# Optimization experiments

Hardware: AMD Instinct MI355X
Metric: run time of the kernel (lower is better)

The kernel has to match this reference:

```python
import jax, jax.numpy as jnp
import numpy as np

N, C, H, W = 8, 32, 48, 48
S, K, OC = 2, 3, 32  # scale_int, kernel_size, out_channels
HID = 256
FEAT = C * K * K  # 288


def setup_inputs() -> dict:
    key = jax.random.key(0)
    ks = jax.random.split(key, 5)
    F_LR = jax.random.normal(ks[0], (N, C, H, W), dtype=jnp.float32)
    v = jax.random.normal(ks[1], (H * S * W * S, 3), dtype=jnp.float32)
    w1 = jax.random.normal(ks[2], (3, HID), dtype=jnp.float32) * 0.2
    b1 = jnp.zeros((HID,), dtype=jnp.float32)
    w2 = jax.random.normal(ks[3], (HID, FEAT * OC), dtype=jnp.float32) * 0.02
    b2 = jnp.zeros((FEAT * OC,), dtype=jnp.float32)
    return {"F_LR": F_LR, "v": v, "w1": w1, "b1": b1, "w2": w2, "b2": b2}


def _unfold(x, k):
    # torch F.unfold(x, k, padding=1): (N, C*k*k, H*W), channel-major then (ki,kj)
    n, c, h, w = x.shape
    xp = jnp.pad(x, ((0, 0), (0, 0), (1, 1), (1, 1)))
    cols = [xp[:, :, i:i + h, j:j + w] for i in range(k) for j in range(k)]
    p = jnp.stack(cols, axis=2)  # (N, C, k*k, H, W)
    return p.reshape(n, c * k * k, h * w)


def reference(F_LR, v, w1, b1, w2, b2):
    n = F_LR.shape[0]
    # weight prediction MLP
    hmid = jax.nn.relu(v @ w1 + b1)
    W_pred = hmid @ w2 + b2  # (H*S*W*S, C*K*K*OC)
    # reshape like torch: view(H,S,W,S,FEAT,OC).permute(1,3,0,2,4,5) -> (S*S, H*W, FEAT, OC)
    Wt = (W_pred.reshape(H, S, W, S, FEAT, OC)
          .transpose(1, 3, 0, 2, 4, 5)
          .reshape(S * S, H * W, FEAT, OC))
    # add_dimensions replicates F_LR S*S times, so patches are shared across p
    pat = _unfold(F_LR, K)  # (N, FEAT, H*W)
    # per-pixel tiny matmul: out[n,p,l,o] = sum_f pat[n,f,l] * Wt[p,l,f,o]
    out = jnp.einsum('nfl,plfo->nplo', pat, Wt)  # (N, S*S, H*W, OC)
    # assemble upsampled image: p=(sh,sw), pixel (h*S+sh, w*S+sw)
    out = (out.reshape(n, S, S, H, W, OC)
           .transpose(0, 5, 3, 1, 4, 2)
           .reshape(n, OC, S * H, S * W))
    # integer scale => create_mask is all-True, masked_select is identity
    return out
```

## Files before the change

### kernel.cpp

```cpp
#include <hip/hip_runtime.h>
#include <hip/hip_bf16.h>

#define NN    8
#define CC    32
#define HH    48
#define WW    48
#define OCC   32
#define HID   256
#define FEAT  288
#define RTOT  9216
#define COLS  9216
#define XUP   96
#define YUP   96
#define OUTSZ (NN*OCC*XUP*YUP)

using bf16x8 = __attribute__((ext_vector_type(8))) __bf16;
using bf16x4 = __attribute__((ext_vector_type(4))) __bf16;
using f32x4  = __attribute__((ext_vector_type(4))) float;

#define GLOAD_LDS16(gp, lp)                                                        \
  __builtin_amdgcn_global_load_lds((const __attribute__((address_space(1))) void*)(gp), \
                                   (__attribute__((address_space(3))) void*)(lp), 16, 0, 0)

__global__ void prep_hmid(const float* __restrict__ v, const float* __restrict__ w1,
                          const float* __restrict__ b1, __hip_bfloat16* __restrict__ hmidp) {
  int r = blockIdx.x;
  int t = threadIdx.x;
  float v0 = v[r*3+0], v1 = v[r*3+1], v2 = v[r*3+2];
  float val = v0*w1[t] + v1*w1[HID+t] + v2*w1[2*HID+t] + b1[t];
  val = fmaxf(val, 0.0f);
  int dst = ((r>>4)*8 + (t>>5))*512 + ((t>>3)&3)*128 + (r&15)*8 + (t&7);
  hmidp[dst] = __float2bfloat16(val);
}

__global__ void prep_w2(const float* __restrict__ w2, __hip_bfloat16* __restrict__ w2p) {
  int idx = blockIdx.x*256 + threadIdx.x;
  int k   = idx / COLS;
  int col = idx % COLS;
  float val = w2[idx];
  int colchunk = col >> 7;
  int cg   = (col >> 4) & 7;
  int lane = (((k>>3)&3)<<4) | (col & 15);
  int kb   = k >> 5;
  int i    = k & 7;
  int dst  = (((colchunk*8 + kb)*8 + cg)*64 + lane)*8 + i;
  w2p[dst] = __float2bfloat16(val);
}

__launch_bounds__(256, 2)
__global__ void fused_main(const float* __restrict__ F_LR,
                           const __hip_bfloat16* __restrict__ hmidp,
                           const __hip_bfloat16* __restrict__ w2p,
                           const float* __restrict__ b2,
                           float* __restrict__ outp,
                           int G, int nch) {
  __shared__ __align__(16) __bf16 pat[CC][3][18][NN];
  __shared__ __align__(16) float  wc[4*OCC*32];
  __shared__ __align__(16) __bf16 Bring[4*4096];
  __shared__ __align__(16) float  biasb[256];
  __shared__ __align__(16) char   dummy[2048];

  const int tid  = threadIdx.x;
  const int lane = tid & 63;
  const int wv   = tid >> 6;
  const int blk  = blockIdx.x;
  int rowtile, g;
  if (G == 2) {
    int xcd = blk & 7;
    int j   = blk >> 3;
    g       = xcd & 1;
    rowtile = (xcd >> 1)*72 + j;
  } else {
    rowtile = blk;
    g       = 0;
  }
  const int X  = rowtile / 3;
  const int Yh = rowtile - X*3;
  const int h  = X >> 1;
  const int w0 = Yh * 16;
  const int l15 = lane & 15;
  const int qt  = lane >> 4;
  const int oc  = lane & 31;
  const int nh  = lane >> 5;
  const int NT = nch*8;

  const char* w2base = (const char*)w2p + (size_t)g*nch*65536;
  char* BringB = (char*)Bring;
  auto stage_any = [&](int t) {
    if (t < NT) {
      const char* src = w2base + (size_t)t*8192 + wv*2048 + lane*16;
      char* dst = BringB + (t&3)*8192 + wv*2048;
      GLOAD_LDS16(src, dst);
      GLOAD_LDS16(src + 1024, dst + 1024);
    } else {
      const char* src = w2base + wv*2048 + lane*16;
      GLOAD_LDS16(src, (char*)dummy);
      GLOAD_LDS16(src + 1024, (char*)dummy + 1024);
    }
  };
  stage_any(0); stage_any(1); stage_any(2);
  asm volatile("" ::: "memory");

  bf16x8 a[2][8];
  {
    const bf16x8* ap = reinterpret_cast<const bf16x8*>(hmidp) + (size_t)rowtile*1024 + lane;
    #pragma unroll
    for (int mg = 0; mg < 2; ++mg)
      #pragma unroll
      for (int kb = 0; kb < 8; ++kb) a[mg][kb] = ap[(mg*8 + kb)*64];
  }

  {
    const int n = tid >> 5, c = tid & 31;
    const float* fsrc = F_LR + ((size_t)(n*CC + c)*HH)*WW;
    #pragma unroll
    for (int ki = 0; ki < 3; ++ki) {
      int hh = h - 1 + ki;
      bool hok = (unsigned)hh < (unsigned)HH;
      #pragma unroll
      for (int wi = 0; wi < 18; ++wi) {
        int ww = w0 - 1 + wi;
        float val = (hok && (unsigned)ww < (unsigned)WW) ? fsrc[hh*WW + ww] : 0.f;
        pat[c][ki][wi][n] = (__bf16)val;
      }
    }
  }
  asm volatile("s_waitcnt lgkmcnt(0)" ::: "memory");
  __builtin_amdgcn_sched_barrier(0);
  __builtin_amdgcn_s_barrier();

  float oacc[8][4];
  #pragma unroll
  for (int i = 0; i < 8; ++i)
    { oacc[i][0]=0.f; oacc[i][1]=0.f; oacc[i][2]=0.f; oacc[i][3]=0.f; }

  for (int ch = 0; ch < nch; ++ch) {
    if ((ch & 1) == 0) {
      const char* bsrc = (const char*)(b2 + (size_t)(g*nch + ch)*128) + lane*16;
      GLOAD_LDS16(bsrc, (char*)biasb);
    }

    f32x4 acc00 = {0,0,0,0}, acc01 = {0,0,0,0}, acc10 = {0,0,0,0}, acc11 = {0,0,0,0};

    #pragma unroll
    for (int s = 0; s < 8; ++s) {
      const int t = ch*8 + s;
      asm volatile("s_waitcnt vmcnt(4)" ::: "memory");
      const char* bufp = BringB + (size_t)(t&3)*8192 + wv*2048;
      bf16x8 b0 = *(const bf16x8*)(bufp + lane*16);
      bf16x8 b1 = *(const bf16x8*)(bufp + 1024 + lane*16);
      stage_any(t + 3);
      acc00 = __builtin_amdgcn_mfma_f32_16x16x32_bf16(a[0][s], b0, acc00, 0,0,0);
      acc01 = __builtin_amdgcn_mfma_f32_16x16x32_bf16(a[0][s], b1, acc01, 0,0,0);
      acc10 = __builtin_amdgcn_mfma_f32_16x16x32_bf16(a[1][s], b0, acc10, 0,0,0);
      acc11 = __builtin_amdgcn_mfma_f32_16x16x32_bf16(a[1][s], b1, acc11, 0,0,0);
    }

    asm volatile("s_waitcnt vmcnt(6)" ::: "memory");
    {
      float bias0 = biasb[(ch&1)*128 + wv*32 + l15];
      float bias1 = biasb[(ch&1)*128 + wv*32 + 16 + l15];
      #pragma unroll
      for (int mg = 0; mg < 2; ++mg) {
        #pragma unroll
        for (int ng = 0; ng < 2; ++ng) {
          f32x4 A = (mg==0) ? (ng==0?acc00:acc01) : (ng==0?acc10:acc11);
          float bb = ng ? bias1 : bias0;
          A[0]+=bb; A[1]+=bb; A[2]+=bb; A[3]+=bb;
          int ocx  = ng*16 + l15;
          int ridx = (mg*16 + qt*4) ^ ((ocx&7)<<2);
          *(f32x4*)&wc[wv*1024 + ocx*32 + ridx] = A;
        }
      }
    }
    asm volatile("s_waitcnt lgkmcnt(0)" ::: "memory");
    __builtin_amdgcn_sched_barrier(0);
    __builtin_amdgcn_s_barrier();

    const int swz = (oc & 7) << 2;
    #pragma unroll
    for (int fl = 0; fl < 4; ++fl) {
      const int f   = (g*nch + ch)*4 + fl;
      const int c   = f / 9;
      const int rem = f - c*9;
      const int ki  = rem / 3;
      const int kj  = rem - ki*3;
      const f32x4 wlo = *(const f32x4*)&wc[fl*1024 + oc*32 + ((wv*8    ) ^ swz)];
      const f32x4 whi = *(const f32x4*)&wc[fl*1024 + oc*32 + ((wv*8 + 4) ^ swz)];
      const __bf16* pbase = &pat[c][ki][0][0] + nh*4;
      #pragma unroll
      for (int rrh = 0; rrh < 4; ++rrh) {
        bf16x4 pq = *(const bf16x4*)(pbase + (wv*4 + rrh + kj)*8);
        float w0v = (rrh < 2) ? ((rrh == 0) ? wlo[0] : wlo[2]) : ((rrh == 2) ? whi[0] : whi[2]);
        float w1v = (rrh < 2) ? ((rrh == 0) ? wlo[1] : wlo[3]) : ((rrh == 2) ? whi[1] : whi[3]);
        #pragma unroll
        for (int q = 0; q < 4; ++q) {
          float pv = (float)pq[q];
          oacc[rrh*2][q]   += w0v * pv;
          oacc[rrh*2+1][q] += w1v * pv;
        }
      }
    }
    asm volatile("s_waitcnt lgkmcnt(0)" ::: "memory");
    __builtin_amdgcn_sched_barrier(0);
    __builtin_amdgcn_s_barrier();
  }

  float* OP = outp + (size_t)g*OUTSZ;
  #pragma unroll
  for (int q = 0; q < 4; ++q) {
    int n = nh*4 + q;
    f32x4 v0, v1;
    v0[0]=oacc[0][q]; v0[1]=oacc[1][q]; v0[2]=oacc[2][q]; v0[3]=oacc[3][q];
    v1[0]=oacc[4][q]; v1[1]=oacc[5][q]; v1[2]=oacc[6][q]; v1[3]=oacc[7][q];
    float* dst = OP + (((size_t)(n*OCC + oc)*XUP + X)*YUP + Yh*32 + wv*8);
    *(f32x4*)dst     = v0;
    *(f32x4*)(dst+4) = v1;
  }
}

__global__ void reduce2(const float* __restrict__ P, float* __restrict__ out) {
  int i = blockIdx.x*256 + threadIdx.x;
  if (i < OUTSZ/4) {
    f32x4 a = ((const f32x4*)P)[i];
    f32x4 b = ((const f32x4*)(P + OUTSZ))[i];
    ((f32x4*)out)[i] = a + b;
  }
}

extern "C" void kernel_launch(void* const* d_in, const int* in_sizes, int n_in,
                              void* d_out, int out_size, void* d_ws, size_t ws_size,
                              hipStream_t stream) {
  const float* F_LR = (const float*)d_in[0];
  const float* v    = (const float*)d_in[1];
  const float* w1   = (const float*)d_in[2];
  const float* b1   = (const float*)d_in[3];
  const float* w2   = (const float*)d_in[4];
  const float* b2   = (const float*)d_in[5];
  float* out = (float*)d_out;

  const size_t prepBytes = (size_t)RTOT*HID*2;
  const size_t need2 = 2*prepBytes + 2ull*OUTSZ*4;
  const int G   = (ws_size >= need2) ? 2 : 1;
  const int nch = 72 / G;

  __hip_bfloat16* hmidp = (__hip_bfloat16*)d_ws;
  __hip_bfloat16* w2p   = (__hip_bfloat16*)((char*)d_ws + prepBytes);
  float* P = (float*)((char*)d_ws + 2*prepBytes);
  float* target = (G == 2) ? P : out;

  hipLaunchKernelGGL(prep_hmid, dim3(RTOT), dim3(HID), 0, stream, v, w1, b1, hmidp);
  hipLaunchKernelGGL(prep_w2,   dim3((HID*COLS)/256), dim3(256), 0, stream, w2, w2p);
  hipLaunchKernelGGL(fused_main, dim3(288*G), dim3(256), 0, stream,
                     F_LR, hmidp, w2p, b2, target, G, nch);
  if (G == 2)
    hipLaunchKernelGGL(reduce2, dim3(OUTSZ/4/256), dim3(256), 0, stream, P, out);
}
```

Baseline: 199.1 us.

## Prefetch w2 tiles directly into registers instead of an LDS ring

Replaces the global_load_lds ring buffer for the w2 B-operand with register double-buffering. Each wave loads its half-chunk of B fragments into VGPRs one chunk ahead, so the MFMAs no longer wait on LDS round trips. The bias slice is now preloaded once into LDS as bf16 instead of being staged per chunk. The shared buffers move to dynamic shared memory. This adds 32 VGPRs of B fragments and so raises register pressure, which could hurt occupancy at 2 waves per SIMD. Rounding the bias to bf16 slightly lowers its precision.

```diff
diff --git a/kernel.cpp b/kernel.cpp
--- a/kernel.cpp
+++ b/kernel.cpp
@@ -18,10 +18,6 @@
 using bf16x4 = __attribute__((ext_vector_type(4))) __bf16;
 using f32x4  = __attribute__((ext_vector_type(4))) float;
 
-#define GLOAD_LDS16(gp, lp)                                                        \
-  __builtin_amdgcn_global_load_lds((const __attribute__((address_space(1))) void*)(gp), \
-                                   (__attribute__((address_space(3))) void*)(lp), 16, 0, 0)
-
 __global__ void prep_hmid(const float* __restrict__ v, const float* __restrict__ w1,
                           const float* __restrict__ b1, __hip_bfloat16* __restrict__ hmidp) {
   int r = blockIdx.x;
@@ -47,6 +43,22 @@
   w2p[dst] = __float2bfloat16(val);
 }
 
+#define BARRIER_LGKM() do {                              \
+    asm volatile("s_waitcnt lgkmcnt(0)" ::: "memory");   \
+    __builtin_amdgcn_sched_barrier(0);                   \
+    __builtin_amdgcn_s_barrier();                        \
+  } while (0)
+
+#define ISSUE_HALF(SET, CH, H) do {                                              \
+    const char* _b = w2base + ((size_t)((CH)*8 + (H)*4))*8192 + wv*2048          \
+                     + (size_t)lane*16;                                          \
+    _Pragma("unroll")                                                            \
+    for (int _i = 0; _i < 4; ++_i) {                                             \
+      SET[0][_i] = *(const bf16x8*)(_b + _i*8192);                               \
+      SET[1][_i] = *(const bf16x8*)(_b + _i*8192 + 1024);                        \
+    }                                                                            \
+  } while (0)
+
 __launch_bounds__(256, 2)
 __global__ void fused_main(const float* __restrict__ F_LR,
                            const __hip_bfloat16* __restrict__ hmidp,
@@ -54,11 +66,10 @@
                            const float* __restrict__ b2,
                            float* __restrict__ outp,
                            int G, int nch) {
-  __shared__ __align__(16) __bf16 pat[CC][3][18][NN];
-  __shared__ __align__(16) float  wc[4*OCC*32];
-  __shared__ __align__(16) __bf16 Bring[4*4096];
-  __shared__ __align__(16) float  biasb[256];
-  __shared__ __align__(16) char   dummy[2048];
+  extern __shared__ __align__(16) char smem[];
+  __bf16* patB  = (__bf16*)smem;
+  float*  wc    = (float*)(smem + 27648);
+  __bf16* biasL = (__bf16*)(smem + 44032);
 
   const int tid  = threadIdx.x;
   const int lane = tid & 63;
@@ -82,24 +93,8 @@
   const int qt  = lane >> 4;
   const int oc  = lane & 31;
   const int nh  = lane >> 5;
-  const int NT = nch*8;
 
   const char* w2base = (const char*)w2p + (size_t)g*nch*65536;
-  char* BringB = (char*)Bring;
-  auto stage_any = [&](int t) {
-    if (t < NT) {
-      const char* src = w2base + (size_t)t*8192 + wv*2048 + lane*16;
-      char* dst = BringB + (t&3)*8192 + wv*2048;
-      GLOAD_LDS16(src, dst);
-      GLOAD_LDS16(src + 1024, dst + 1024);
-    } else {
-      const char* src = w2base + wv*2048 + lane*16;
-      GLOAD_LDS16(src, (char*)dummy);
-      GLOAD_LDS16(src + 1024, (char*)dummy + 1024);
-    }
-  };
-  stage_any(0); stage_any(1); stage_any(2);
-  asm volatile("" ::: "memory");
 
   bf16x8 a[2][8];
   {
@@ -110,6 +105,9 @@
       for (int kb = 0; kb < 8; ++kb) a[mg][kb] = ap[(mg*8 + kb)*64];
   }
 
+  for (int i = tid; i < nch*128; i += 256)
+    biasL[i] = (__bf16)b2[g*nch*128 + i];
+
   {
     const int n = tid >> 5, c = tid & 31;
     const float* fsrc = F_LR + ((size_t)(n*CC + c)*HH)*WW;
@@ -121,45 +119,45 @@
       for (int wi = 0; wi < 18; ++wi) {
         int ww = w0 - 1 + wi;
         float val = (hok && (unsigned)ww < (unsigned)WW) ? fsrc[hh*WW + ww] : 0.f;
-        pat[c][ki][wi][n] = (__bf16)val;
+        patB[((c*3 + ki)*18 + wi)*8 + n] = (__bf16)val;
       }
     }
   }
-  asm volatile("s_waitcnt lgkmcnt(0)" ::: "memory");
-  __builtin_amdgcn_sched_barrier(0);
-  __builtin_amdgcn_s_barrier();
+  BARRIER_LGKM();
 
   float oacc[8][4];
   #pragma unroll
   for (int i = 0; i < 8; ++i)
     { oacc[i][0]=0.f; oacc[i][1]=0.f; oacc[i][2]=0.f; oacc[i][3]=0.f; }
 
+  bf16x8 bA[2][4], bB[2][4];
+  ISSUE_HALF(bA, 0, 0);
+  ISSUE_HALF(bB, 0, 1);
+
   for (int ch = 0; ch < nch; ++ch) {
-    if ((ch & 1) == 0) {
-      const char* bsrc = (const char*)(b2 + (size_t)(g*nch + ch)*128) + lane*16;
-      GLOAD_LDS16(bsrc, (char*)biasb);
-    }
-
     f32x4 acc00 = {0,0,0,0}, acc01 = {0,0,0,0}, acc10 = {0,0,0,0}, acc11 = {0,0,0,0};
 
     #pragma unroll
-    for (int s = 0; s < 8; ++s) {
-      const int t = ch*8 + s;
-      asm volatile("s_waitcnt vmcnt(4)" ::: "memory");
-      const char* bufp = BringB + (size_t)(t&3)*8192 + wv*2048;
-      bf16x8 b0 = *(const bf16x8*)(bufp + lane*16);
-      bf16x8 b1 = *(const bf16x8*)(bufp + 1024 + lane*16);
-      stage_any(t + 3);
-      acc00 = __builtin_amdgcn_mfma_f32_16x16x32_bf16(a[0][s], b0, acc00, 0,0,0);
-      acc01 = __builtin_amdgcn_mfma_f32_16x16x32_bf16(a[0][s], b1, acc01, 0,0,0);
-      acc10 = __builtin_amdgcn_mfma_f32_16x16x32_bf16(a[1][s], b0, acc10, 0,0,0);
-      acc11 = __builtin_amdgcn_mfma_f32_16x16x32_bf16(a[1][s], b1, acc11, 0,0,0);
-    }
-
-    asm volatile("s_waitcnt vmcnt(6)" ::: "memory");
+    for (int s = 0; s < 4; ++s) {
+      acc00 = __builtin_amdgcn_mfma_f32_16x16x32_bf16(a[0][s], bA[0][s], acc00, 0,0,0);
+      acc01 = __builtin_amdgcn_mfma_f32_16x16x32_bf16(a[0][s], bA[1][s], acc01, 0,0,0);
+      acc10 = __builtin_amdgcn_mfma_f32_16x16x32_bf16(a[1][s], bA[0][s], acc10, 0,0,0);
+      acc11 = __builtin_amdgcn_mfma_f32_16x16x32_bf16(a[1][s], bA[1][s], acc11, 0,0,0);
+    }
+    if (ch + 1 < nch) { ISSUE_HALF(bA, ch+1, 0); }
+
+    #pragma unroll
+    for (int s = 0; s < 4; ++s) {
+      acc00 = __builtin_amdgcn_mfma_f32_16x16x32_bf16(a[0][4+s], bB[0][s], acc00, 0,0,0);
+      acc01 = __builtin_amdgcn_mfma_f32_16x16x32_bf16(a[0][4+s], bB[1][s], acc01, 0,0,0);
+      acc10 = __builtin_amdgcn_mfma_f32_16x16x32_bf16(a[1][4+s], bB[0][s], acc10, 0,0,0);
+      acc11 = __builtin_amdgcn_mfma_f32_16x16x32_bf16(a[1][4+s], bB[1][s], acc11, 0,0,0);
+    }
+    if (ch + 1 < nch) { ISSUE_HALF(bB, ch+1, 1); }
+
     {
-      float bias0 = biasb[(ch&1)*128 + wv*32 + l15];
-      float bias1 = biasb[(ch&1)*128 + wv*32 + 16 + l15];
+      float bias0 = (float)biasL[ch*128 + wv*32 + l15];
+      float bias1 = (float)biasL[ch*128 + wv*32 + 16 + l15];
       #pragma unroll
       for (int mg = 0; mg < 2; ++mg) {
         #pragma unroll
@@ -173,9 +171,7 @@
         }
       }
     }
-    asm volatile("s_waitcnt lgkmcnt(0)" ::: "memory");
-    __builtin_amdgcn_sched_barrier(0);
-    __builtin_amdgcn_s_barrier();
+    BARRIER_LGKM();
 
     const int swz = (oc & 7) << 2;
     #pragma unroll
@@ -187,7 +183,7 @@
       const int kj  = rem - ki*3;
       const f32x4 wlo = *(const f32x4*)&wc[fl*1024 + oc*32 + ((wv*8    ) ^ swz)];
       const f32x4 whi = *(const f32x4*)&wc[fl*1024 + oc*32 + ((wv*8 + 4) ^ swz)];
-      const __bf16* pbase = &pat[c][ki][0][0] + nh*4;
+      const __bf16* pbase = patB + (c*3 + ki)*18*8 + nh*4;
       #pragma unroll
       for (int rrh = 0; rrh < 4; ++rrh) {
         bf16x4 pq = *(const bf16x4*)(pbase + (wv*4 + rrh + kj)*8);
@@ -201,9 +197,7 @@
         }
       }
     }
-    asm volatile("s_waitcnt lgkmcnt(0)" ::: "memory");
-    __builtin_amdgcn_sched_barrier(0);
-    __builtin_amdgcn_s_barrier();
+    BARRIER_LGKM();
   }
 
   float* OP = outp + (size_t)g*OUTSZ;
@@ -249,9 +243,11 @@
   float* P = (float*)((char*)d_ws + 2*prepBytes);
   float* target = (G == 2) ? P : out;
 
+  const size_t shmem = 27648 + 16384 + (size_t)nch*128*2;
+
   hipLaunchKernelGGL(prep_hmid, dim3(RTOT), dim3(HID), 0, stream, v, w1, b1, hmidp);
   hipLaunchKernelGGL(prep_w2,   dim3((HID*COLS)/256), dim3(256), 0, stream, w2, w2p);
-  hipLaunchKernelGGL(fused_main, dim3(288*G), dim3(256), 0, stream,
+  hipLaunchKernelGGL(fused_main, dim3(288*G), dim3(256), shmem, stream,
                      F_LR, hmidp, w2p, b2, target, G, nch);
   if (G == 2)
     hipLaunchKernelGGL(reduce2, dim3(OUTSZ/4/256), dim3(256), 0, stream, P, out);
```

After: 176.1 us. -11.5%, faster.
